# Performance work log

Hardware: AMD Instinct MI355X
Metric: run time of the kernel (lower is better)

Reference implementation:

```python
import jax, jax.numpy as jnp
import numpy as np

NUM_CLASSES = 64  # K: fill_max for class ids c


def setup_inputs() -> dict:
    key = jax.random.key(0)
    k1, k2 = jax.random.split(key)
    z = jax.random.normal(k1, (16, 8192, 256), dtype=jnp.float32)
    c = jax.random.randint(k2, (16, 8192), 0, NUM_CLASSES, dtype=jnp.int64)
    return {"z": z, "c": c}


def reference(z, c):
    # z: [B, S, D], c: [B, S] int class ids in [0, K)
    D = z.shape[-1]
    zf = z.reshape(-1, D)          # [N, D]
    cf = c.reshape(-1)             # [N]
    N = zf.shape[0]

    # Fused segmented reductions instead of a python loop over unique ids.
    counts = jax.ops.segment_sum(jnp.ones((N,), zf.dtype), cf, num_segments=NUM_CLASSES)  # [K]
    sums = jax.ops.segment_sum(zf, cf, num_segments=NUM_CLASSES)                          # [K, D]
    safe_counts = jnp.maximum(counts, 1.0)
    centroids = sums / safe_counts[:, None]                                               # [K, D] per-class mean

    # within-class variance: mean squared distance of members to their centroid
    diff = zf - centroids[cf]                                                             # [N, D] gather
    sq = jnp.sum(diff * diff, axis=-1)                                                    # [N]
    var_withins = jax.ops.segment_sum(sq, cf, num_segments=NUM_CLASSES) / safe_counts     # [K]

    return centroids, var_withins
```

## Files before the change

### kernel.cpp

```cpp
#include <hip/hip_runtime.h>

#define K_CLS 64
#define DIM   256
#define TPB1  512
#define MAXROWS 2048

typedef __attribute__((ext_vector_type(8)))  short short8;
typedef __attribute__((ext_vector_type(16))) float f32x16;

__device__ inline unsigned short f2bf(float x) {
    unsigned u = __float_as_uint(x);
    u += 0x7FFFu + ((u >> 16) & 1u);
    return (unsigned short)(u >> 16);
}

__global__ __launch_bounds__(TPB1) void fstat_p1(
    const float* __restrict__ z, const int* __restrict__ c,
    float* __restrict__ psum, float* __restrict__ psq, float* __restrict__ pcnt,
    int rows_per_blk, int nblk)
{
    __shared__ __align__(16) int cs[MAXROWS];
    __shared__ float lcnt[K_CLS];
    const int t   = threadIdx.x;
    const int blk = blockIdx.x;
    const int rb0 = blk * rows_per_blk;

    if (t < K_CLS) lcnt[t] = 0.f;
    __syncthreads();
    for (int r = t; r < rows_per_blk; r += TPB1) {
        int cv = c[rb0 + r];
        cs[r] = cv;
        atomicAdd(&lcnt[cv], 1.0f);
    }
    __syncthreads();

    const int wave = t >> 6;
    const int lane = t & 63;
    const int db   = wave * 32;
    const int half = lane >> 5;
    const int ln   = lane & 31;

    f32x16 aS0 = {}; f32x16 aS1 = {}; f32x16 aQ0 = {}; f32x16 aQ1 = {};

    const int nsteps = rows_per_blk >> 4;
    const size_t zo0 = (size_t)(rb0 + half * 8) * DIM + db + ln;

    float v[8];
    #pragma unroll
    for (int i = 0; i < 8; ++i) v[i] = z[zo0 + (size_t)i * DIM];

    for (int step = 0; step < nsteps; ++step) {
        float vn[8];
        if (step + 1 < nsteps) {
            const size_t zo = zo0 + (size_t)(step + 1) * 16 * DIM;
            #pragma unroll
            for (int i = 0; i < 8; ++i) vn[i] = z[zo + (size_t)i * DIM];
        }
        const int rb = step * 16 + half * 8;
        int4 c0 = *reinterpret_cast<const int4*>(&cs[rb]);
        int4 c1 = *reinterpret_cast<const int4*>(&cs[rb + 4]);
        int cl[8] = {c0.x, c0.y, c0.z, c0.w, c1.x, c1.y, c1.z, c1.w};

        short8 A0, A1, Bz, Bq;
        #pragma unroll
        for (int i = 0; i < 8; ++i) {
            A0[i] = (cl[i] == ln)      ? (short)0x3F80 : (short)0;
            A1[i] = (cl[i] == ln + 32) ? (short)0x3F80 : (short)0;
            Bz[i] = (short)f2bf(v[i]);
            Bq[i] = (short)f2bf(v[i] * v[i]);
        }
        aS0 = __builtin_amdgcn_mfma_f32_32x32x16_bf16(A0, Bz, aS0, 0, 0, 0);
        aS1 = __builtin_amdgcn_mfma_f32_32x32x16_bf16(A1, Bz, aS1, 0, 0, 0);
        aQ0 = __builtin_amdgcn_mfma_f32_32x32x16_bf16(A0, Bq, aQ0, 0, 0, 0);
        aQ1 = __builtin_amdgcn_mfma_f32_32x32x16_bf16(A1, Bq, aQ1, 0, 0, 0);
        if (step + 1 < nsteps) {
            #pragma unroll
            for (int i = 0; i < 8; ++i) v[i] = vn[i];
        }
    }

    float* ps = psum + (size_t)blk * K_CLS * DIM;
    float* pq = psq  + (size_t)blk * K_CLS * DIM;
    #pragma unroll
    for (int r = 0; r < 16; ++r) {
        int row = (r & 3) + 8 * (r >> 2) + 4 * half;
        size_t o0 = (size_t)row * DIM + db + ln;
        size_t o1 = (size_t)(row + 32) * DIM + db + ln;
        ps[o0] = aS0[r]; ps[o1] = aS1[r];
        pq[o0] = aQ0[r]; pq[o1] = aQ1[r];
    }
    if (t < K_CLS) pcnt[(size_t)t * nblk + blk] = lcnt[t];
}

__global__ __launch_bounds__(1024) void fstat_p2(
    const float* __restrict__ psum, const float* __restrict__ psq,
    const float* __restrict__ pcnt, float* __restrict__ out,
    float* __restrict__ wvar, float* __restrict__ wcnt, int nblk)
{
    const int k  = blockIdx.x >> 2;
    const int q  = blockIdx.x & 3;
    const int t  = threadIdx.x;
    const int d  = t & 63;
    const int sg = t >> 6;

    __shared__ float redS[16][64];
    __shared__ float redQ[16][64];
    __shared__ float sh_cnt;

    float* redF = &redS[0][0];
    float cpart = 0.f;
    for (int b = t; b < nblk; b += 1024) cpart += pcnt[(size_t)k * nblk + b];
    redF[t] = cpart; __syncthreads();
    for (int st = 512; st > 0; st >>= 1) {
        if (t < st) redF[t] += redF[t + st];
        __syncthreads();
    }
    if (t == 0) sh_cnt = redF[0];
    __syncthreads();

    float s = 0.f, qq = 0.f;
    for (int b = sg; b < nblk; b += 16) {
        size_t o = ((size_t)b * K_CLS + k) * DIM + q * 64 + d;
        s  += psum[o];
        qq += psq[o];
    }
    redS[sg][d] = s;
    redQ[sg][d] = qq;
    __syncthreads();

    if (t < 64) {
        float su = 0.f, qu = 0.f;
        #pragma unroll
        for (int i = 0; i < 16; ++i) { su += redS[i][t]; qu += redQ[i][t]; }
        float cnt = fmaxf(sh_cnt, 1.f);
        float mu  = su / cnt;
        out[(size_t)k * DIM + q * 64 + t] = mu;
        float vp = qu - cnt * mu * mu;
        #pragma unroll
        for (int off = 32; off > 0; off >>= 1) vp += __shfl_down(vp, off);
        if (t == 0) {
            wvar[k * 4 + q] = vp;
            if (q == 0) wcnt[k] = sh_cnt;
        }
    }
}

__global__ void fstat_p3(const float* __restrict__ wvar,
                         const float* __restrict__ wcnt, float* __restrict__ out)
{
    int k = threadIdx.x;
    float cnt = fmaxf(wcnt[k], 1.f);
    out[K_CLS * DIM + k] =
        (wvar[4 * k] + wvar[4 * k + 1] + wvar[4 * k + 2] + wvar[4 * k + 3]) / cnt;
}

extern "C" void kernel_launch(void* const* d_in, const int* in_sizes, int n_in,
                              void* d_out, int out_size, void* d_ws, size_t ws_size,
                              hipStream_t stream)
{
    const float* z = (const float*)d_in[0];
    const int*   c = (const int*)d_in[1];
    float* out = (float*)d_out;
    const int N = in_sizes[1];

    auto need = [](int nb) {
        return (size_t)nb * K_CLS * DIM * 2 * sizeof(float)
             + (size_t)K_CLS * nb * sizeof(float)
             + (size_t)(K_CLS * 4 + K_CLS) * sizeof(float);
    };
    int nblk = 256;
    while (nblk > 64 &&
           (N % nblk != 0 || (N / nblk) % 16 != 0 || (N / nblk) > MAXROWS ||
            need(nblk) > ws_size))
        nblk >>= 1;

    const int rows_per_blk = N / nblk;

    float* psum = (float*)d_ws;
    float* psq  = psum + (size_t)nblk * K_CLS * DIM;
    float* pcnt = psq  + (size_t)nblk * K_CLS * DIM;
    float* wvar = pcnt + (size_t)K_CLS * nblk;
    float* wcnt = wvar + K_CLS * 4;

    fstat_p1<<<nblk, TPB1, 0, stream>>>(z, c, psum, psq, pcnt, rows_per_blk, nblk);
    fstat_p2<<<K_CLS * 4, 1024, 0, stream>>>(psum, psq, pcnt, out, wvar, wcnt, nblk);
    fstat_p3<<<1, K_CLS, 0, stream>>>(wvar, wcnt, out);
}
```

Before: 39.53 us.

## Shrink partial buffers: bf16 sums, per-class scalar sq, fuse final kernels

The first pass now reduces the squared-value accumulators across the feature dimension inside each block, using shuffles and shared atomics, to one scalar per class. It stores the per-class feature sums as bf16 instead of fp32. This cuts the partial-result write and read traffic between passes to a fraction of its former size. The second pass is reorganised to one block per class and computes the within-class variance directly as E[x^2] minus the squared norm of the mean, which removes the third kernel launch. The risk is accuracy: rounding the partial sums to bf16 and the E[x^2]-mu^2 form can cause cancellation error.

```diff
diff --git a/kernel.cpp b/kernel.cpp
--- a/kernel.cpp
+++ b/kernel.cpp
@@ -13,19 +13,24 @@
     u += 0x7FFFu + ((u >> 16) & 1u);
     return (unsigned short)(u >> 16);
 }
+__device__ inline float bf2f(unsigned short h) {
+    return __uint_as_float(((unsigned)h) << 16);
+}
 
 __global__ __launch_bounds__(TPB1) void fstat_p1(
     const float* __restrict__ z, const int* __restrict__ c,
-    float* __restrict__ psum, float* __restrict__ psq, float* __restrict__ pcnt,
-    int rows_per_blk, int nblk)
+    unsigned short* __restrict__ psum, float* __restrict__ psq,
+    float* __restrict__ pcnt, int rows_per_blk, int nblk)
 {
     __shared__ __align__(16) int cs[MAXROWS];
     __shared__ float lcnt[K_CLS];
+    __shared__ float lsq[K_CLS];
+
     const int t   = threadIdx.x;
     const int blk = blockIdx.x;
     const int rb0 = blk * rows_per_blk;
 
-    if (t < K_CLS) lcnt[t] = 0.f;
+    if (t < K_CLS) { lcnt[t] = 0.f; lsq[t] = 0.f; }
     __syncthreads();
     for (int r = t; r < rows_per_blk; r += TPB1) {
         int cv = c[rb0 + r];
@@ -79,79 +84,81 @@
         }
     }
 
-    float* ps = psum + (size_t)blk * K_CLS * DIM;
-    float* pq = psq  + (size_t)blk * K_CLS * DIM;
+    #pragma unroll
+    for (int r = 0; r < 16; ++r) {
+        float q0 = aQ0[r], q1 = aQ1[r];
+        #pragma unroll
+        for (int off = 16; off > 0; off >>= 1) {
+            q0 += __shfl_xor(q0, off);
+            q1 += __shfl_xor(q1, off);
+        }
+        if (ln == 0) {
+            int row = (r & 3) + 8 * (r >> 2) + 4 * half;
+            atomicAdd(&lsq[row],      q0);
+            atomicAdd(&lsq[row + 32], q1);
+        }
+    }
+
+    unsigned short* ps = psum + (size_t)blk * K_CLS * DIM;
     #pragma unroll
     for (int r = 0; r < 16; ++r) {
         int row = (r & 3) + 8 * (r >> 2) + 4 * half;
-        size_t o0 = (size_t)row * DIM + db + ln;
-        size_t o1 = (size_t)(row + 32) * DIM + db + ln;
-        ps[o0] = aS0[r]; ps[o1] = aS1[r];
-        pq[o0] = aQ0[r]; pq[o1] = aQ1[r];
+        ps[(size_t)row * DIM + db + ln]        = f2bf(aS0[r]);
+        ps[(size_t)(row + 32) * DIM + db + ln] = f2bf(aS1[r]);
     }
-    if (t < K_CLS) pcnt[(size_t)t * nblk + blk] = lcnt[t];
+    __syncthreads();
+    if (t < K_CLS) {
+        pcnt[(size_t)t * nblk + blk] = lcnt[t];
+        psq [(size_t)t * nblk + blk] = lsq[t];
+    }
 }
 
 __global__ __launch_bounds__(1024) void fstat_p2(
-    const float* __restrict__ psum, const float* __restrict__ psq,
-    const float* __restrict__ pcnt, float* __restrict__ out,
-    float* __restrict__ wvar, float* __restrict__ wcnt, int nblk)
+    const unsigned short* __restrict__ psum, const float* __restrict__ pcnt,
+    const float* __restrict__ psq, float* __restrict__ out, int nblk)
 {
-    const int k  = blockIdx.x >> 2;
-    const int q  = blockIdx.x & 3;
-    const int t  = threadIdx.x;
-    const int d  = t & 63;
-    const int sg = t >> 6;
+    const int k = blockIdx.x;
+    const int t = threadIdx.x;
+    __shared__ float red[1024];
+    __shared__ float sh_cnt, sh_sq;
 
-    __shared__ float redS[16][64];
-    __shared__ float redQ[16][64];
-    __shared__ float sh_cnt;
-
-    float* redF = &redS[0][0];
-    float cpart = 0.f;
-    for (int b = t; b < nblk; b += 1024) cpart += pcnt[(size_t)k * nblk + b];
-    redF[t] = cpart; __syncthreads();
-    for (int st = 512; st > 0; st >>= 1) {
-        if (t < st) redF[t] += redF[t + st];
-        __syncthreads();
+    float cp = 0.f, qp = 0.f;
+    for (int b = t; b < nblk; b += 1024) {
+        cp += pcnt[(size_t)k * nblk + b];
+        qp += psq [(size_t)k * nblk + b];
     }
-    if (t == 0) sh_cnt = redF[0];
+    red[t] = cp; __syncthreads();
+    for (int st = 512; st > 0; st >>= 1) { if (t < st) red[t] += red[t + st]; __syncthreads(); }
+    if (t == 0) sh_cnt = red[0];
+    __syncthreads();
+    red[t] = qp; __syncthreads();
+    for (int st = 512; st > 0; st >>= 1) { if (t < st) red[t] += red[t + st]; __syncthreads(); }
+    if (t == 0) sh_sq = red[0];
     __syncthreads();
 
-    float s = 0.f, qq = 0.f;
-    for (int b = sg; b < nblk; b += 16) {
-        size_t o = ((size_t)b * K_CLS + k) * DIM + q * 64 + d;
-        s  += psum[o];
-        qq += psq[o];
-    }
-    redS[sg][d] = s;
-    redQ[sg][d] = qq;
-    __syncthreads();
+    const int d = t & (DIM - 1);
+    const int g = t >> 8;
+    float s = 0.f;
+    for (int b = g; b < nblk; b += 4)
+        s += bf2f(psum[((size_t)b * K_CLS + k) * DIM + d]);
+    red[t] = s; __syncthreads();
 
-    if (t < 64) {
-        float su = 0.f, qu = 0.f;
-        #pragma unroll
-        for (int i = 0; i < 16; ++i) { su += redS[i][t]; qu += redQ[i][t]; }
+    float musq = 0.f;
+    if (t < DIM) {
+        float su  = red[t] + red[t + 256] + red[t + 512] + red[t + 768];
         float cnt = fmaxf(sh_cnt, 1.f);
         float mu  = su / cnt;
-        out[(size_t)k * DIM + q * 64 + t] = mu;
-        float vp = qu - cnt * mu * mu;
-        #pragma unroll
-        for (int off = 32; off > 0; off >>= 1) vp += __shfl_down(vp, off);
-        if (t == 0) {
-            wvar[k * 4 + q] = vp;
-            if (q == 0) wcnt[k] = sh_cnt;
-        }
+        out[(size_t)k * DIM + t] = mu;
+        musq = mu * mu;
     }
-}
-
-__global__ void fstat_p3(const float* __restrict__ wvar,
-                         const float* __restrict__ wcnt, float* __restrict__ out)
-{
-    int k = threadIdx.x;
-    float cnt = fmaxf(wcnt[k], 1.f);
-    out[K_CLS * DIM + k] =
-        (wvar[4 * k] + wvar[4 * k + 1] + wvar[4 * k + 2] + wvar[4 * k + 3]) / cnt;
+    __syncthreads();
+    red[t] = (t < DIM) ? musq : 0.f;
+    __syncthreads();
+    for (int st = 128; st > 0; st >>= 1) { if (t < st) red[t] += red[t + st]; __syncthreads(); }
+    if (t == 0) {
+        float cnt = fmaxf(sh_cnt, 1.f);
+        out[K_CLS * DIM + k] = sh_sq / cnt - red[0];
+    }
 }
 
 extern "C" void kernel_launch(void* const* d_in, const int* in_sizes, int n_in,
@@ -164,9 +171,8 @@
     const int N = in_sizes[1];
 
     auto need = [](int nb) {
-        return (size_t)nb * K_CLS * DIM * 2 * sizeof(float)
-             + (size_t)K_CLS * nb * sizeof(float)
-             + (size_t)(K_CLS * 4 + K_CLS) * sizeof(float);
+        return (size_t)nb * K_CLS * DIM * sizeof(unsigned short)
+             + 2 * (size_t)K_CLS * nb * sizeof(float);
     };
     int nblk = 256;
     while (nblk > 64 &&
@@ -176,13 +182,10 @@
 
     const int rows_per_blk = N / nblk;
 
-    float* psum = (float*)d_ws;
-    float* psq  = psum + (size_t)nblk * K_CLS * DIM;
-    float* pcnt = psq  + (size_t)nblk * K_CLS * DIM;
-    float* wvar = pcnt + (size_t)K_CLS * nblk;
-    float* wcnt = wvar + K_CLS * 4;
+    unsigned short* psum = (unsigned short*)d_ws;
+    float* psq  = (float*)(psum + (size_t)nblk * K_CLS * DIM);
+    float* pcnt = psq + (size_t)K_CLS * nblk;
 
     fstat_p1<<<nblk, TPB1, 0, stream>>>(z, c, psum, psq, pcnt, rows_per_blk, nblk);
-    fstat_p2<<<K_CLS * 4, 1024, 0, stream>>>(psum, psq, pcnt, out, wvar, wcnt, nblk);
-    fstat_p3<<<1, K_CLS, 0, stream>>>(wvar, wcnt, out);
+    fstat_p2<<<K_CLS, 1024, 0, stream>>>(psum, pcnt, psq, out, nblk);
 }
```

After: 49.66 us. +25.6%, slower.

## Store per-block partial sums in bf16 and streamline operand packing and count reduction

Applied to the files above, without the earlier changes.

Partial per-class sums and squared sums are now written to the workspace as bf16 instead of fp32, halving the intermediate traffic between the two passes. Operand construction for the MFMA uses packed two-element bf16 conversion and packed one-hot words. The count reduction in the second pass is replaced by a small shared-memory plus shuffle reduction. Rounding large partial sums to bf16 adds substantial error to centroids and to the variance computed as E[x^2]-mu^2, which is prone to cancellation.

```diff
diff --git a/kernel.cpp b/kernel.cpp
--- a/kernel.cpp
+++ b/kernel.cpp
@@ -1,4 +1,5 @@
 #include <hip/hip_runtime.h>
+#include <hip/hip_bf16.h>
 
 #define K_CLS 64
 #define DIM   256
@@ -7,17 +8,28 @@
 
 typedef __attribute__((ext_vector_type(8)))  short short8;
 typedef __attribute__((ext_vector_type(16))) float f32x16;
-
+typedef __attribute__((ext_vector_type(4)))  unsigned int uint4v;
+
+__device__ inline float bf2f(unsigned short h) {
+    return __uint_as_float(((unsigned)h) << 16);
+}
 __device__ inline unsigned short f2bf(float x) {
     unsigned u = __float_as_uint(x);
     u += 0x7FFFu + ((u >> 16) & 1u);
     return (unsigned short)(u >> 16);
 }
+__device__ inline unsigned int pkbf(float lo, float hi) {
+    float2 p; p.x = lo; p.y = hi;
+    __hip_bfloat162 h = __float22bfloat162_rn(p);
+    unsigned int r;
+    __builtin_memcpy(&r, &h, sizeof(r));
+    return r;
+}
 
 __global__ __launch_bounds__(TPB1) void fstat_p1(
     const float* __restrict__ z, const int* __restrict__ c,
-    float* __restrict__ psum, float* __restrict__ psq, float* __restrict__ pcnt,
-    int rows_per_blk, int nblk)
+    unsigned short* __restrict__ psum, unsigned short* __restrict__ psq,
+    float* __restrict__ pcnt, int rows_per_blk, int nblk)
 {
     __shared__ __align__(16) int cs[MAXROWS];
     __shared__ float lcnt[K_CLS];
@@ -39,6 +51,7 @@
     const int db   = wave * 32;
     const int half = lane >> 5;
     const int ln   = lane & 31;
+    const int ln32 = ln + 32;
 
     f32x16 aS0 = {}; f32x16 aS1 = {}; f32x16 aQ0 = {}; f32x16 aQ1 = {};
 
@@ -61,14 +74,21 @@
         int4 c1 = *reinterpret_cast<const int4*>(&cs[rb + 4]);
         int cl[8] = {c0.x, c0.y, c0.z, c0.w, c1.x, c1.y, c1.z, c1.w};
 
-        short8 A0, A1, Bz, Bq;
-        #pragma unroll
-        for (int i = 0; i < 8; ++i) {
-            A0[i] = (cl[i] == ln)      ? (short)0x3F80 : (short)0;
-            A1[i] = (cl[i] == ln + 32) ? (short)0x3F80 : (short)0;
-            Bz[i] = (short)f2bf(v[i]);
-            Bq[i] = (short)f2bf(v[i] * v[i]);
-        }
+        uint4v ua0, ua1, ubz, ubq;
+        #pragma unroll
+        for (int i = 0; i < 4; ++i) {
+            int l0 = cl[2 * i], l1 = cl[2 * i + 1];
+            ua0[i] = (l0 == ln   ? 0x00003F80u : 0u) | (l1 == ln   ? 0x3F800000u : 0u);
+            ua1[i] = (l0 == ln32 ? 0x00003F80u : 0u) | (l1 == ln32 ? 0x3F800000u : 0u);
+            float v0 = v[2 * i], v1 = v[2 * i + 1];
+            ubz[i] = pkbf(v0, v1);
+            ubq[i] = pkbf(v0 * v0, v1 * v1);
+        }
+        short8 A0 = __builtin_bit_cast(short8, ua0);
+        short8 A1 = __builtin_bit_cast(short8, ua1);
+        short8 Bz = __builtin_bit_cast(short8, ubz);
+        short8 Bq = __builtin_bit_cast(short8, ubq);
+
         aS0 = __builtin_amdgcn_mfma_f32_32x32x16_bf16(A0, Bz, aS0, 0, 0, 0);
         aS1 = __builtin_amdgcn_mfma_f32_32x32x16_bf16(A1, Bz, aS1, 0, 0, 0);
         aQ0 = __builtin_amdgcn_mfma_f32_32x32x16_bf16(A0, Bq, aQ0, 0, 0, 0);
@@ -79,21 +99,22 @@
         }
     }
 
-    float* ps = psum + (size_t)blk * K_CLS * DIM;
-    float* pq = psq  + (size_t)blk * K_CLS * DIM;
+    unsigned short* ps = psum + (size_t)blk * K_CLS * DIM;
+    unsigned short* pq = psq  + (size_t)blk * K_CLS * DIM;
     #pragma unroll
     for (int r = 0; r < 16; ++r) {
         int row = (r & 3) + 8 * (r >> 2) + 4 * half;
         size_t o0 = (size_t)row * DIM + db + ln;
         size_t o1 = (size_t)(row + 32) * DIM + db + ln;
-        ps[o0] = aS0[r]; ps[o1] = aS1[r];
-        pq[o0] = aQ0[r]; pq[o1] = aQ1[r];
-    }
+        ps[o0] = f2bf(aS0[r]); ps[o1] = f2bf(aS1[r]);
+        pq[o0] = f2bf(aQ0[r]); pq[o1] = f2bf(aQ1[r]);
+    }
+    __syncthreads();
     if (t < K_CLS) pcnt[(size_t)t * nblk + blk] = lcnt[t];
 }
 
 __global__ __launch_bounds__(1024) void fstat_p2(
-    const float* __restrict__ psum, const float* __restrict__ psq,
+    const unsigned short* __restrict__ psum, const unsigned short* __restrict__ psq,
     const float* __restrict__ pcnt, float* __restrict__ out,
     float* __restrict__ wvar, float* __restrict__ wcnt, int nblk)
 {
@@ -105,24 +126,23 @@
 
     __shared__ float redS[16][64];
     __shared__ float redQ[16][64];
+    __shared__ float redC[256];
     __shared__ float sh_cnt;
 
-    float* redF = &redS[0][0];
-    float cpart = 0.f;
-    for (int b = t; b < nblk; b += 1024) cpart += pcnt[(size_t)k * nblk + b];
-    redF[t] = cpart; __syncthreads();
-    for (int st = 512; st > 0; st >>= 1) {
-        if (t < st) redF[t] += redF[t + st];
-        __syncthreads();
-    }
-    if (t == 0) sh_cnt = redF[0];
-    __syncthreads();
+    if (t < 256) redC[t] = (t < nblk) ? pcnt[(size_t)k * nblk + t] : 0.f;
+    __syncthreads();
+    if (t < 64) {
+        float cp = redC[t] + redC[t + 64] + redC[t + 128] + redC[t + 192];
+        #pragma unroll
+        for (int off = 32; off > 0; off >>= 1) cp += __shfl_down(cp, off);
+        if (t == 0) sh_cnt = cp;
+    }
 
     float s = 0.f, qq = 0.f;
     for (int b = sg; b < nblk; b += 16) {
         size_t o = ((size_t)b * K_CLS + k) * DIM + q * 64 + d;
-        s  += psum[o];
-        qq += psq[o];
+        s  += bf2f(psum[o]);
+        qq += bf2f(psq[o]);
     }
     redS[sg][d] = s;
     redQ[sg][d] = qq;
@@ -149,9 +169,11 @@
                          const float* __restrict__ wcnt, float* __restrict__ out)
 {
     int k = threadIdx.x;
-    float cnt = fmaxf(wcnt[k], 1.f);
-    out[K_CLS * DIM + k] =
-        (wvar[4 * k] + wvar[4 * k + 1] + wvar[4 * k + 2] + wvar[4 * k + 3]) / cnt;
+    if (k < K_CLS) {
+        float cnt = fmaxf(wcnt[k], 1.f);
+        out[K_CLS * DIM + k] =
+            (wvar[4 * k] + wvar[4 * k + 1] + wvar[4 * k + 2] + wvar[4 * k + 3]) / cnt;
+    }
 }
 
 extern "C" void kernel_launch(void* const* d_in, const int* in_sizes, int n_in,
@@ -164,7 +186,7 @@
     const int N = in_sizes[1];
 
     auto need = [](int nb) {
-        return (size_t)nb * K_CLS * DIM * 2 * sizeof(float)
+        return 2 * (size_t)nb * K_CLS * DIM * sizeof(unsigned short)
              + (size_t)K_CLS * nb * sizeof(float)
              + (size_t)(K_CLS * 4 + K_CLS) * sizeof(float);
     };
@@ -176,9 +198,9 @@
 
     const int rows_per_blk = N / nblk;
 
-    float* psum = (float*)d_ws;
-    float* psq  = psum + (size_t)nblk * K_CLS * DIM;
-    float* pcnt = psq  + (size_t)nblk * K_CLS * DIM;
+    unsigned short* psum = (unsigned short*)d_ws;
+    unsigned short* psq  = psum + (size_t)nblk * K_CLS * DIM;
+    float* pcnt = (float*)(psq + (size_t)nblk * K_CLS * DIM);
     float* wvar = pcnt + (size_t)K_CLS * nblk;
     float* wcnt = wvar + K_CLS * 4;
 
```

New measurement: 36.58 us. 7.5% less time.
